# Performance work log

Hardware: AMD Instinct MI355X
Metric: run time of the kernel (lower is better)

Reference implementation:

```python
import jax, jax.numpy as jnp
import numpy as np
import math

B, T, C, H = 4, 1024, 1024, 16
D = C // H  # head dim = 64

def setup_inputs() -> dict:
    key = jax.random.key(0)
    ks = jax.random.split(key, 10)
    s = 1.0 / math.sqrt(C)
    x = jax.random.normal(ks[0], (B, T, C), dtype=jnp.float32)
    pad = (jax.random.uniform(ks[1], (B, T)) < 0.2).astype(jnp.float32)
    # ensure first token of every row is unpadded so softmax rows are well-posed
    pad = pad.at[:, 0].set(0.0)
    Wq = jax.random.normal(ks[2], (C, C), dtype=jnp.float32) * s
    bq = jnp.zeros((C,), dtype=jnp.float32)
    Wk = jax.random.normal(ks[3], (C, C), dtype=jnp.float32) * s
    bk = jnp.zeros((C,), dtype=jnp.float32)
    Wv = jax.random.normal(ks[4], (C, C), dtype=jnp.float32) * s
    bv = jnp.zeros((C,), dtype=jnp.float32)
    Wp = jax.random.normal(ks[5], (C, C), dtype=jnp.float32) * s
    bp = jnp.zeros((C,), dtype=jnp.float32)
    return {"x": x, "x_padding_judge": pad, "Wq": Wq, "bq": bq,
            "Wk": Wk, "bk": bk, "Wv": Wv, "bv": bv, "Wp": Wp, "bp": bp}

def reference(x, x_padding_judge, Wq, bq, Wk, bk, Wv, bv, Wp, bp):
    # keep flag: 1.0 where token is real, 0.0 where padded
    keep = 1.0 - x_padding_judge                      # [B, T]
    mask = keep[:, :, None] * keep[:, None, :]        # [B, T, T] outer product
    # projections, split heads: [B, H, T, D]
    def heads(w, b):
        return (x @ w + b).reshape(B, T, H, D).transpose(0, 2, 1, 3)
    q, k, v = heads(Wq, bq), heads(Wk, bk), heads(Wv, bv)
    att = jnp.einsum('bhqd,bhkd->bhqk', q, k) * (1.0 / math.sqrt(D))
    # attn_pdrop=0 => att_full is all ones; masked_fill where mask == 0
    att = jnp.where(mask[:, None, :, :] == 0, -1e9, att)
    att = jax.nn.softmax(att, axis=-1)
    y = jnp.einsum('bhqk,bhkd->bhqd', att, v)         # [B, H, T, D]
    y = y.transpose(0, 2, 1, 3).reshape(B, T, C)
    return y @ Wp + bp
```

## Files before the change

kernel.cpp:

```cpp
#include <hip/hip_runtime.h>
#include <hip/hip_bf16.h>
#include <math.h>

#define Bb 4
#define Tt 1024
#define Cc 1024
#define Hh 16
#define Dd 64

typedef __attribute__((ext_vector_type(8))) _Float16 half8;
typedef __attribute__((ext_vector_type(4))) _Float16 half4;
typedef __attribute__((ext_vector_type(4))) float floatx4;


__device__ __forceinline__ void gload_lds16(const _Float16* g, const _Float16* l)
{
    __builtin_amdgcn_global_load_lds(
        (const __attribute__((address_space(1))) void*)g,
        (__attribute__((address_space(3))) void*)l, 16, 0, 0);
}

struct PrepP { const float* x; _Float16* xh; const float* W[4]; _Float16* out[4]; };

__global__ __launch_bounds__(256) void prep_all(PrepP p)
{
    if (blockIdx.x < 256) {
        const int m16 = blockIdx.x;
        const int r   = threadIdx.x & 15;
        const int kc0 = threadIdx.x >> 4;
        const float* src = p.x + (size_t)(m16 * 16 + r) * 1024;
        _Float16*   dst = p.xh + (size_t)m16 * 16384 + r * 8;
#pragma unroll
        for (int c8 = 0; c8 < 8; ++c8) {
            const int kc = kc0 + c8 * 16;
            float4 a = *(const float4*)(src + kc * 8);
            float4 b = *(const float4*)(src + kc * 8 + 4);
            half8 h;
            h[0] = (_Float16)a.x; h[1] = (_Float16)a.y; h[2] = (_Float16)a.z; h[3] = (_Float16)a.w;
            h[4] = (_Float16)b.x; h[5] = (_Float16)b.y; h[6] = (_Float16)b.z; h[7] = (_Float16)b.w;
            *(half8*)(dst + kc * 128) = h;
        }
        return;
    }
    const int bid2 = blockIdx.x - 256;
    const int z    = bid2 >> 8;
    const int rem  = bid2 & 255;
    const int n0   = (rem & 15) * 64;
    const int k0   = (rem >> 4) * 64;
    const float* __restrict__ W = p.W[z];
    _Float16* __restrict__ outp = p.out[z];
    __shared__ float tile[64][65];
    const int tr  = threadIdx.x >> 4;
    const int tc4 = (threadIdx.x & 15) * 4;

#pragma unroll
    for (int i = 0; i < 4; ++i) {
        const int kk = tr + i * 16;
        float4 v = *(const float4*)(W + (size_t)(k0 + kk) * 1024 + n0 + tc4);
        tile[kk][tc4 + 0] = v.x;
        tile[kk][tc4 + 1] = v.y;
        tile[kk][tc4 + 2] = v.z;
        tile[kk][tc4 + 3] = v.w;
    }
    __syncthreads();
#pragma unroll
    for (int i = 0; i < 4; ++i) {
        half4 h;
#pragma unroll
        for (int c = 0; c < 4; ++c) h[c] = (_Float16)tile[tc4 + c][tr + i * 16];
        _Float16* dst = outp + (size_t)((n0 >> 4) + i) * 16384
                        + ((k0 + tc4) >> 3) * 128 + tr * 8 + (tc4 & 7);
        *(half4*)dst = h;
    }
}

struct QkvP { const _Float16* Wt[3]; const float* bias[3];
              _Float16* qb; _Float16* kb; _Float16* vt; };

#define QKV_STEP(CUR, SBUF, TS, DOSTAGE, TAILWAIT)                          \
    {                                                                       \
        half8 af[2], bf[4];                                                 \
        _Pragma("unroll")                                                   \
        for (int i = 0; i < 2; ++i)                                         \
            af[i] = *(const half8*)&As[CUR][wr * 2 + i][lane * 8];          \
        _Pragma("unroll")                                                   \
        for (int j = 0; j < 4; ++j)                                         \
            bf[j] = *(const half8*)&Bs[CUR][wc * 4 + j][lane * 8];          \
        if (DOSTAGE) {                                                      \
            const size_t ko = (size_t)(TS) * 512;                           \
            gload_lds16(ga + ko, &As[SBUF][w][0]);                          \
            gload_lds16(gb + ko, &Bs[SBUF][w][0]);                          \
        }                                                                   \
        _Pragma("unroll")                                                   \
        for (int i = 0; i < 2; ++i)                                         \
            _Pragma("unroll")                                               \
            for (int j = 0; j < 4; ++j)                                     \
                acc[i][j] = __builtin_amdgcn_mfma_f32_16x16x32_f16(         \
                    af[i], bf[j], acc[i][j], 0, 0, 0);                      \
        if ((TAILWAIT) == 2)                                                \
            asm volatile("s_waitcnt vmcnt(2)" ::: "memory");                \
        else if ((TAILWAIT) == 0)                                           \
            asm volatile("s_waitcnt vmcnt(0)" ::: "memory");                \
        if ((TAILWAIT) >= 0) __builtin_amdgcn_s_barrier();                  \
    }

__global__ __launch_bounds__(512) void gemm_qkv(const _Float16* __restrict__ xh, QkvP p)
{
    const int z = blockIdx.z;
    const _Float16* __restrict__ Wt   = p.Wt[z];
    const float* __restrict__    bias = p.bias[z];

    const int tid  = threadIdx.x;
    const int lane = tid & 63;
    const int w    = tid >> 6;
    const int wr   = w >> 1, wc = w & 1;
    const int quad = lane >> 4;
    const int l15  = lane & 15;
    const int bm   = blockIdx.x * 128;
    const int bn   = blockIdx.y * 128;

    __shared__ __align__(16) _Float16 As[3][8][512];
    __shared__ __align__(16) _Float16 Bs[3][8][512];

    const _Float16* ga = xh + (size_t)((bm >> 4) + w) * 16384 + lane * 8;
    const _Float16* gb = Wt + (size_t)((bn >> 4) + w) * 16384 + lane * 8;

    floatx4 acc[2][4];
#pragma unroll
    for (int i = 0; i < 2; ++i)
#pragma unroll
        for (int j = 0; j < 4; ++j)
            acc[i][j] = (floatx4){0.f, 0.f, 0.f, 0.f};

    gload_lds16(ga, &As[0][w][0]);
    gload_lds16(gb, &Bs[0][w][0]);
    gload_lds16(ga + 512, &As[1][w][0]);
    gload_lds16(gb + 512, &Bs[1][w][0]);
    asm volatile("s_waitcnt vmcnt(2)" ::: "memory");
    __builtin_amdgcn_s_barrier();

    for (int tt = 0; tt < 30; tt += 3) {
        QKV_STEP(0, 2, tt + 2, true, 2);
        QKV_STEP(1, 0, tt + 3, true, 2);
        QKV_STEP(2, 1, tt + 4, true, 2);
    }
    QKV_STEP(0, 0, 0, false, 0);
    QKV_STEP(1, 0, 0, false, -1);

    if (z == 2) {
#pragma unroll
        for (int j = 0; j < 4; ++j) {
            const int col = bn + wc * 64 + j * 16 + l15;
            const int h  = col >> 6;
            const float bj = bias[col];
#pragma unroll
            for (int i = 0; i < 2; ++i) {
                const int t0 = bm + wr * 32 + i * 16 + quad * 4;
                const int bh = (t0 >> 10) * 16 + h;
                const int tm = t0 & 1023;
                half4 pk;
#pragma unroll
                for (int r = 0; r < 4; ++r) pk[r] = (_Float16)(acc[i][j][r] + bj);
                *(half4*)(p.vt + (size_t)bh * 65536 + (size_t)j * 16384
                          + (tm >> 3) * 128 + l15 * 8 + (tm & 7)) = pk;
            }
        }
    } else {
        _Float16* outp = (z == 0) ? p.qb : p.kb;
#pragma unroll
        for (int j = 0; j < 4; ++j) {
            const int col = bn + wc * 64 + j * 16 + l15;
            const int h  = col >> 6;
            const int dd = col & 63;
            const float bj = bias[col];
            const int doff = (dd >> 3) * 128 + (dd & 7);
#pragma unroll
            for (int i = 0; i < 2; ++i) {
#pragma unroll
                for (int r = 0; r < 4; ++r) {
                    const int tg = bm + wr * 32 + i * 16 + quad * 4 + r;
                    const int bh = (tg >> 10) * 16 + h;
                    const int tm = tg & 1023;
                    outp[(size_t)bh * 65536 + (tm >> 4) * 1024 + doff + (tm & 15) * 8] =
                        (_Float16)(acc[i][j][r] + bj);
                }
            }
        }
    }
}

#define ATTN_TILE(AKC, BVC, AKN, BVN, KTC, KTN, DOLOAD)                     \
    {                                                                       \
        if (DOLOAD) {                                                       \
            _Pragma("unroll")                                               \
            for (int ks = 0; ks < 2; ++ks) {                                \
                _Pragma("unroll")                                           \
                for (int mk = 0; mk < 4; ++mk)                              \
                    AKN[ks][mk] = *(const half8*)(kf                        \
                        + (size_t)(((KTN) >> 4) + mk) * 1024                \
                        + ks * 512 + lane * 8);                             \
                _Pragma("unroll")                                           \
                for (int dj = 0; dj < 4; ++dj)                              \
                    BVN[ks][dj] = *(const half8*)(vf + (size_t)dj * 16384   \
                        + ((KTN) >> 3) * 128 + ks * 512 + lane * 8);        \
            }                                                               \
        }                                                                   \
        float4 kk4[4];                                                      \
        _Pragma("unroll")                                                   \
        for (int mk = 0; mk < 4; ++mk)                                      \
            kk4[mk] = *(const float4*)&Pad[(KTC) + mk * 16 + quad * 4];     \
        floatx4 ST[4][2];                                                   \
        _Pragma("unroll")                                                   \
        for (int mk = 0; mk < 4; ++mk)                                      \
            _Pragma("unroll")                                               \
            for (int nq = 0; nq < 2; ++nq)                                  \
                ST[mk][nq] = (floatx4){0.f, 0.f, 0.f, 0.f};                 \
        _Pragma("unroll")                                                   \
        for (int ks = 0; ks < 2; ++ks)                                      \
            _Pragma("unroll")                                               \
            for (int mk = 0; mk < 4; ++mk)                                  \
                _Pragma("unroll")                                           \
                for (int nq = 0; nq < 2; ++nq)                              \
                    ST[mk][nq] = __builtin_amdgcn_mfma_f32_16x16x32_f16(    \
                        AKC[ks][mk], bq[ks][nq], ST[mk][nq], 0, 0, 0);      \
        _Pragma("unroll")                                                   \
        for (int mk = 0; mk < 4; ++mk) {                                    \
            const float kkr[4] = {1.0f - kk4[mk].x, 1.0f - kk4[mk].y,       \
                                  1.0f - kk4[mk].z, 1.0f - kk4[mk].w};      \
            _Pragma("unroll")                                               \
            for (int nq = 0; nq < 2; ++nq) {                                \
                half4 pk;                                                   \
                _Pragma("unroll")                                           \
                for (int r = 0; r < 4; ++r) {                               \
                    const float e = __builtin_amdgcn_exp2f(ST[mk][nq][r] * SC); \
                    const float pv = (kq[nq] == 0.0f) ? 1.0f : kkr[r] * e;  \
                    pk[r] = (_Float16)pv;                                   \
                }                                                           \
                *(half4*)&Ps[w][((mk * 2 + (quad >> 1)) * 32 + nq * 16 + l15) * 8 \
                               + (quad & 1) * 4] = pk;                      \
            }                                                               \
        }                                                                   \
        _Pragma("unroll")                                                   \
        for (int ks = 0; ks < 2; ++ks) {                                    \
            half8 ap[2];                                                    \
            _Pragma("unroll")                                               \
            for (int mi = 0; mi < 2; ++mi)                                  \
                ap[mi] = *(const half8*)&Ps[w][((ks * 4 + quad) * 32 + mi * 16 + l15) * 8]; \
            _Pragma("unroll")                                               \
            for (int mi = 0; mi < 2; ++mi) {                                \
                _Pragma("unroll")                                           \
                for (int dj = 0; dj < 4; ++dj)                              \
                    O[mi][dj] = __builtin_amdgcn_mfma_f32_16x16x32_f16(     \
                        ap[mi], BVC[ks][dj], O[mi][dj], 0, 0, 0);           \
                l_acc[mi] = __builtin_amdgcn_mfma_f32_16x16x32_f16(         \
                    ap[mi], ones, l_acc[mi], 0, 0, 0);                      \
            }                                                               \
        }                                                                   \
    }

__global__ __launch_bounds__(256) void attn_mfma(
    const _Float16* __restrict__ qb, const _Float16* __restrict__ kb,
    const _Float16* __restrict__ vt, const float* __restrict__ padj,
    _Float16* __restrict__ yh)
{
    __shared__ __align__(16) _Float16 Ps[4][2048];
    __shared__ __align__(16) float    Pad[1024];

    const int tid  = threadIdx.x;
    const int lane = tid & 63;
    const int w    = tid >> 6;
    const int quad = lane >> 4;
    const int l15  = lane & 15;
    const int bh   = blockIdx.x;
    const int q0   = blockIdx.y * 128;
    const int b    = bh >> 4;
    const int h    = bh & 15;

    const _Float16* qf = qb + (size_t)bh * 65536;
    const _Float16* kf = kb + (size_t)bh * 65536;
    const _Float16* vf = vt + (size_t)bh * 65536;
    const float*    pk_row = padj + b * Tt;

    *(float4*)&Pad[tid * 4] = *(const float4*)(pk_row + tid * 4);

    half8 bq[2][2];
#pragma unroll
    for (int ks = 0; ks < 2; ++ks)
#pragma unroll
        for (int nq = 0; nq < 2; ++nq)
            bq[ks][nq] = *(const half8*)(qf + (size_t)((q0 >> 4) + w * 2 + nq) * 1024
                                         + ks * 512 + lane * 8);
    float kq[2];
#pragma unroll
    for (int nq = 0; nq < 2; ++nq)
        kq[nq] = 1.0f - pk_row[q0 + w * 32 + nq * 16 + l15];

    floatx4 O[2][4];
    floatx4 l_acc[2];
#pragma unroll
    for (int mi = 0; mi < 2; ++mi) {
#pragma unroll
        for (int dj = 0; dj < 4; ++dj) O[mi][dj] = (floatx4){0.f, 0.f, 0.f, 0.f};
        l_acc[mi] = (floatx4){0.f, 0.f, 0.f, 0.f};
    }
    half8 ones;
#pragma unroll
    for (int j = 0; j < 8; ++j) ones[j] = (_Float16)1.0f;

    constexpr float SC = 0.18033688011112042f;

    __syncthreads();

    half8 ak0[2][4], bv0[2][4], ak1[2][4], bv1[2][4];
#pragma unroll
    for (int ks = 0; ks < 2; ++ks) {
#pragma unroll
        for (int mk = 0; mk < 4; ++mk)
            ak0[ks][mk] = *(const half8*)(kf + (size_t)mk * 1024 + ks * 512 + lane * 8);
#pragma unroll
        for (int dj = 0; dj < 4; ++dj)
            bv0[ks][dj] = *(const half8*)(vf + (size_t)dj * 16384 + ks * 512 + lane * 8);
    }

    for (int tt = 0; tt < 896; tt += 128) {
        ATTN_TILE(ak0, bv0, ak1, bv1, tt, tt + 64, true);
        ATTN_TILE(ak1, bv1, ak0, bv0, tt + 64, tt + 128, true);
    }
    ATTN_TILE(ak0, bv0, ak1, bv1, 896, 960, true);
    ATTN_TILE(ak1, bv1, ak0, bv0, 960, 0, false);

#pragma unroll
    for (int mi = 0; mi < 2; ++mi) {
#pragma unroll
        for (int r = 0; r < 4; ++r) {
            const int rowl  = w * 32 + mi * 16 + quad * 4 + r;
            const int token = b * Tt + q0 + rowl;
            const float inv = 1.0f / l_acc[mi][r];
            const size_t tb = (size_t)(token >> 4) * 16384 + (token & 15) * 8;
#pragma unroll
            for (int dj = 0; dj < 4; ++dj) {
                const int col = h * 64 + dj * 16 + l15;
                yh[tb + (col >> 3) * 128 + (col & 7)] = (_Float16)(O[mi][dj][r] * inv);
            }
        }
    }
}

#define PROJ_STEP(CUR, SBUF, TS, DOSTAGE, TAILWAIT)                         \
    {                                                                       \
        half8 af[2], bf[4];                                                 \
        _Pragma("unroll")                                                   \
        for (int i = 0; i < 2; ++i)                                         \
            af[i] = *(const half8*)&As[CUR][wr * 2 + i][lane * 8];          \
        _Pragma("unroll")                                                   \
        for (int j = 0; j < 4; ++j)                                         \
            bf[j] = *(const half8*)&Bs[CUR][wc * 4 + j][lane * 8];          \
        if (DOSTAGE) {                                                      \
            const size_t ko = (size_t)(TS) * 512;                           \
            gload_lds16(ga + ko, &As[SBUF][w][0]);                          \
            gload_lds16(gb + ko, &Bs[SBUF][w][0]);                          \
        }                                                                   \
        _Pragma("unroll")                                                   \
        for (int i = 0; i < 2; ++i)                                         \
            _Pragma("unroll")                                               \
            for (int j = 0; j < 4; ++j)                                     \
                acc[i][j] = __builtin_amdgcn_mfma_f32_16x16x32_f16(         \
                    af[i], bf[j], acc[i][j], 0, 0, 0);                      \
        if ((TAILWAIT) == 6)                                                \
            asm volatile("s_waitcnt vmcnt(6)" ::: "memory");                \
        else if ((TAILWAIT) == 4)                                           \
            asm volatile("s_waitcnt vmcnt(4)" ::: "memory");                \
        else if ((TAILWAIT) == 2)                                           \
            asm volatile("s_waitcnt vmcnt(2)" ::: "memory");                \
        else if ((TAILWAIT) == 0)                                           \
            asm volatile("s_waitcnt vmcnt(0)" ::: "memory");                \
        if ((TAILWAIT) >= 0) __builtin_amdgcn_s_barrier();                  \
    }

__global__ __launch_bounds__(512) void gemm_proj(const _Float16* __restrict__ Ay,
                                                 const _Float16* __restrict__ Bt,
                                                 const float* __restrict__ bias,
                                                 float* __restrict__ out)
{
    const int tid  = threadIdx.x;
    const int lane = tid & 63;
    const int w    = tid >> 6;
    const int wr   = w >> 1, wc = w & 1;
    const int quad = lane >> 4;
    const int l15  = lane & 15;
    const int bm   = blockIdx.x * 128;
    const int bn   = blockIdx.y * 128;

    __shared__ __align__(16) _Float16 As[5][8][512];
    __shared__ __align__(16) _Float16 Bs[5][8][512];

    const _Float16* ga = Ay + (size_t)((bm >> 4) + w) * 16384 + lane * 8;
    const _Float16* gb = Bt + (size_t)((bn >> 4) + w) * 16384 + lane * 8;

    floatx4 acc[2][4];
#pragma unroll
    for (int i = 0; i < 2; ++i)
#pragma unroll
        for (int j = 0; j < 4; ++j)
            acc[i][j] = (floatx4){0.f, 0.f, 0.f, 0.f};

#pragma unroll
    for (int tb = 0; tb < 4; ++tb) {
        gload_lds16(ga + (size_t)tb * 512, &As[tb][w][0]);
        gload_lds16(gb + (size_t)tb * 512, &Bs[tb][w][0]);
    }
    asm volatile("s_waitcnt vmcnt(6)" ::: "memory");
    __builtin_amdgcn_s_barrier();

    for (int tt = 0; tt < 25; tt += 5) {
        PROJ_STEP(0, 4, tt + 4, true, 6);
        PROJ_STEP(1, 0, tt + 5, true, 6);
        PROJ_STEP(2, 1, tt + 6, true, 6);
        PROJ_STEP(3, 2, tt + 7, true, 6);
        PROJ_STEP(4, 3, tt + 8, true, 6);
    }
    PROJ_STEP(0, 4, 29, true, 6);
    PROJ_STEP(1, 0, 30, true, 6);
    PROJ_STEP(2, 1, 31, true, 6);
    PROJ_STEP(3, 0, 0, false, 4);
    PROJ_STEP(4, 0, 0, false, 2);
    PROJ_STEP(0, 0, 0, false, 0);
    PROJ_STEP(1, 0, 0, false, -1);

#pragma unroll
    for (int j = 0; j < 4; ++j) {
        const int col = bn + wc * 64 + j * 16 + l15;
        const float bj = bias[col];
#pragma unroll
        for (int i = 0; i < 2; ++i) {
            const int row = bm + wr * 32 + i * 16 + quad * 4;
            float* o = out + (size_t)row * 1024 + col;
#pragma unroll
            for (int r = 0; r < 4; ++r)
                o[(size_t)r * 1024] = acc[i][j][r] + bj;
        }
    }
}

extern "C" void kernel_launch(void* const* d_in, const int* in_sizes, int n_in,
                              void* d_out, int out_size, void* d_ws, size_t ws_size,
                              hipStream_t stream)
{
    const float* x    = (const float*)d_in[0];
    const float* padj = (const float*)d_in[1];
    const float* Wq   = (const float*)d_in[2];
    const float* bq   = (const float*)d_in[3];
    const float* Wk   = (const float*)d_in[4];
    const float* bk   = (const float*)d_in[5];
    const float* Wv   = (const float*)d_in[6];
    const float* bv   = (const float*)d_in[7];
    const float* Wp   = (const float*)d_in[8];
    const float* bp   = (const float*)d_in[9];
    float* out = (float*)d_out;

    const size_t MB = 1024 * 1024;
    char* ws = (char*)d_ws;
    _Float16* xh  = (_Float16*)(ws);
    _Float16* Wt0 = (_Float16*)(ws +  8 * MB);
    _Float16* Wt1 = (_Float16*)(ws + 10 * MB);
    _Float16* Wt2 = (_Float16*)(ws + 12 * MB);
    _Float16* Wtp = (_Float16*)(ws + 14 * MB);
    _Float16* qb  = (_Float16*)(ws + 16 * MB);
    _Float16* kb  = (_Float16*)(ws + 24 * MB);
    _Float16* vtb = (_Float16*)(ws + 32 * MB);
    _Float16* yh  = (_Float16*)(ws + 40 * MB);

    PrepP pp;
    pp.x = x; pp.xh = xh;
    pp.W[0] = Wq; pp.W[1] = Wk; pp.W[2] = Wv; pp.W[3] = Wp;
    pp.out[0] = Wt0; pp.out[1] = Wt1; pp.out[2] = Wt2; pp.out[3] = Wtp;
    prep_all<<<1280, 256, 0, stream>>>(pp);

    QkvP qp;
    qp.Wt[0] = Wt0; qp.Wt[1] = Wt1; qp.Wt[2] = Wt2;
    qp.bias[0] = bq; qp.bias[1] = bk; qp.bias[2] = bv;
    qp.qb = qb; qp.kb = kb; qp.vt = vtb;
    gemm_qkv<<<dim3(32, 8, 3), 512, 0, stream>>>(xh, qp);

    attn_mfma<<<dim3(64, 8), 256, 0, stream>>>(qb, kb, vtb, padj, yh);

    gemm_proj<<<dim3(32, 8), 512, 0, stream>>>(yh, Wtp, bp, out);
}
```

Baseline: 176.2 us.

## Halve attention query tile per wave to 16 rows and double the grid

Each wave in the attention kernel now handles 16 query rows instead of 32, so the block covers 64 queries and the grid doubles to 1024 blocks. Accumulator registers and LDS for P are halved, and launch bounds request 3 blocks per SM to raise occupancy and spread work across CUs. The cost is that every K/V fragment loaded from global memory is reused across half as many queries, doubling K/V traffic and per-tile overhead such as the exp/mask work per MFMA.

```diff
diff --git a/kernel.cpp b/kernel.cpp
--- a/kernel.cpp
+++ b/kernel.cpp
@@ -209,61 +209,48 @@
         _Pragma("unroll")                                                   \
         for (int mk = 0; mk < 4; ++mk)                                      \
             kk4[mk] = *(const float4*)&Pad[(KTC) + mk * 16 + quad * 4];     \
-        floatx4 ST[4][2];                                                   \
+        floatx4 ST[4];                                                      \
         _Pragma("unroll")                                                   \
         for (int mk = 0; mk < 4; ++mk)                                      \
-            _Pragma("unroll")                                               \
-            for (int nq = 0; nq < 2; ++nq)                                  \
-                ST[mk][nq] = (floatx4){0.f, 0.f, 0.f, 0.f};                 \
+            ST[mk] = (floatx4){0.f, 0.f, 0.f, 0.f};                         \
         _Pragma("unroll")                                                   \
         for (int ks = 0; ks < 2; ++ks)                                      \
             _Pragma("unroll")                                               \
             for (int mk = 0; mk < 4; ++mk)                                  \
-                _Pragma("unroll")                                           \
-                for (int nq = 0; nq < 2; ++nq)                              \
-                    ST[mk][nq] = __builtin_amdgcn_mfma_f32_16x16x32_f16(    \
-                        AKC[ks][mk], bq[ks][nq], ST[mk][nq], 0, 0, 0);      \
+                ST[mk] = __builtin_amdgcn_mfma_f32_16x16x32_f16(            \
+                    AKC[ks][mk], bq[ks], ST[mk], 0, 0, 0);                  \
         _Pragma("unroll")                                                   \
         for (int mk = 0; mk < 4; ++mk) {                                    \
             const float kkr[4] = {1.0f - kk4[mk].x, 1.0f - kk4[mk].y,       \
                                   1.0f - kk4[mk].z, 1.0f - kk4[mk].w};      \
-            _Pragma("unroll")                                               \
-            for (int nq = 0; nq < 2; ++nq) {                                \
-                half4 pk;                                                   \
-                _Pragma("unroll")                                           \
-                for (int r = 0; r < 4; ++r) {                               \
-                    const float e = __builtin_amdgcn_exp2f(ST[mk][nq][r] * SC); \
-                    const float pv = (kq[nq] == 0.0f) ? 1.0f : kkr[r] * e;  \
-                    pk[r] = (_Float16)pv;                                   \
-                }                                                           \
-                *(half4*)&Ps[w][((mk * 2 + (quad >> 1)) * 32 + nq * 16 + l15) * 8 \
-                               + (quad & 1) * 4] = pk;                      \
+            half4 pk;                                                       \
+            _Pragma("unroll")                                               \
+            for (int r = 0; r < 4; ++r) {                                   \
+                const float e = __builtin_amdgcn_exp2f(ST[mk][r] * SC);     \
+                const float pv = (kq == 0.0f) ? 1.0f : kkr[r] * e;          \
+                pk[r] = (_Float16)pv;                                       \
             }                                                               \
+            *(half4*)&Ps[w][((mk * 2 + (quad >> 1)) * 16 + l15) * 8         \
+                           + (quad & 1) * 4] = pk;                          \
         }                                                                   \
         _Pragma("unroll")                                                   \
         for (int ks = 0; ks < 2; ++ks) {                                    \
-            half8 ap[2];                                                    \
-            _Pragma("unroll")                                               \
-            for (int mi = 0; mi < 2; ++mi)                                  \
-                ap[mi] = *(const half8*)&Ps[w][((ks * 4 + quad) * 32 + mi * 16 + l15) * 8]; \
-            _Pragma("unroll")                                               \
-            for (int mi = 0; mi < 2; ++mi) {                                \
-                _Pragma("unroll")                                           \
-                for (int dj = 0; dj < 4; ++dj)                              \
-                    O[mi][dj] = __builtin_amdgcn_mfma_f32_16x16x32_f16(     \
-                        ap[mi], BVC[ks][dj], O[mi][dj], 0, 0, 0);           \
-                l_acc[mi] = __builtin_amdgcn_mfma_f32_16x16x32_f16(         \
-                    ap[mi], ones, l_acc[mi], 0, 0, 0);                      \
-            }                                                               \
+            half8 ap = *(const half8*)&Ps[w][((ks * 4 + quad) * 16 + l15) * 8]; \
+            _Pragma("unroll")                                               \
+            for (int dj = 0; dj < 4; ++dj)                                  \
+                O[dj] = __builtin_amdgcn_mfma_f32_16x16x32_f16(             \
+                    ap, BVC[ks][dj], O[dj], 0, 0, 0);                       \
+            l_acc = __builtin_amdgcn_mfma_f32_16x16x32_f16(                 \
+                ap, ones, l_acc, 0, 0, 0);                                  \
         }                                                                   \
     }
 
-__global__ __launch_bounds__(256) void attn_mfma(
+__global__ __launch_bounds__(256, 3) void attn_mfma(
     const _Float16* __restrict__ qb, const _Float16* __restrict__ kb,
     const _Float16* __restrict__ vt, const float* __restrict__ padj,
     _Float16* __restrict__ yh)
 {
-    __shared__ __align__(16) _Float16 Ps[4][2048];
+    __shared__ __align__(16) _Float16 Ps[4][1024];
     __shared__ __align__(16) float    Pad[1024];
 
     const int tid  = threadIdx.x;
@@ -272,7 +259,7 @@
     const int quad = lane >> 4;
     const int l15  = lane & 15;
     const int bh   = blockIdx.x;
-    const int q0   = blockIdx.y * 128;
+    const int q0   = blockIdx.y * 64;
     const int b    = bh >> 4;
     const int h    = bh & 15;
 
@@ -283,26 +270,18 @@
 
     *(float4*)&Pad[tid * 4] = *(const float4*)(pk_row + tid * 4);
 
-    half8 bq[2][2];
+    half8 bq[2];
 #pragma unroll
     for (int ks = 0; ks < 2; ++ks)
-#pragma unroll
-        for (int nq = 0; nq < 2; ++nq)
-            bq[ks][nq] = *(const half8*)(qf + (size_t)((q0 >> 4) + w * 2 + nq) * 1024
-                                         + ks * 512 + lane * 8);
-    float kq[2];
-#pragma unroll
-    for (int nq = 0; nq < 2; ++nq)
-        kq[nq] = 1.0f - pk_row[q0 + w * 32 + nq * 16 + l15];
-
-    floatx4 O[2][4];
-    floatx4 l_acc[2];
-#pragma unroll
-    for (int mi = 0; mi < 2; ++mi) {
-#pragma unroll
-        for (int dj = 0; dj < 4; ++dj) O[mi][dj] = (floatx4){0.f, 0.f, 0.f, 0.f};
-        l_acc[mi] = (floatx4){0.f, 0.f, 0.f, 0.f};
-    }
+        bq[ks] = *(const half8*)(qf + (size_t)((q0 >> 4) + w) * 1024
+                                 + ks * 512 + lane * 8);
+    const float kq = 1.0f - pk_row[q0 + w * 16 + l15];
+
+    floatx4 O[4];
+    floatx4 l_acc;
+#pragma unroll
+    for (int dj = 0; dj < 4; ++dj) O[dj] = (floatx4){0.f, 0.f, 0.f, 0.f};
+    l_acc = (floatx4){0.f, 0.f, 0.f, 0.f};
     half8 ones;
 #pragma unroll
     for (int j = 0; j < 8; ++j) ones[j] = (_Float16)1.0f;
@@ -330,18 +309,15 @@
     ATTN_TILE(ak1, bv1, ak0, bv0, 960, 0, false);
 
 #pragma unroll
-    for (int mi = 0; mi < 2; ++mi) {
-#pragma unroll
-        for (int r = 0; r < 4; ++r) {
-            const int rowl  = w * 32 + mi * 16 + quad * 4 + r;
-            const int token = b * Tt + q0 + rowl;
-            const float inv = 1.0f / l_acc[mi][r];
-            const size_t tb = (size_t)(token >> 4) * 16384 + (token & 15) * 8;
-#pragma unroll
-            for (int dj = 0; dj < 4; ++dj) {
-                const int col = h * 64 + dj * 16 + l15;
-                yh[tb + (col >> 3) * 128 + (col & 7)] = (_Float16)(O[mi][dj][r] * inv);
-            }
+    for (int r = 0; r < 4; ++r) {
+        const int rowl  = w * 16 + quad * 4 + r;
+        const int token = b * Tt + q0 + rowl;
+        const float inv = 1.0f / l_acc[r];
+        const size_t tb = (size_t)(token >> 4) * 16384 + (token & 15) * 8;
+#pragma unroll
+        for (int dj = 0; dj < 4; ++dj) {
+            const int col = h * 64 + dj * 16 + l15;
+            yh[tb + (col >> 3) * 128 + (col & 7)] = (_Float16)(O[dj][r] * inv);
         }
     }
 }
@@ -482,7 +458,7 @@
     qp.qb = qb; qp.kb = kb; qp.vt = vtb;
     gemm_qkv<<<dim3(32, 8, 3), 512, 0, stream>>>(xh, qp);
 
-    attn_mfma<<<dim3(64, 8), 256, 0, stream>>>(qb, kb, vtb, padj, yh);
+    attn_mfma<<<dim3(64, 16), 256, 0, stream>>>(qb, kb, vtb, padj, yh);
 
     gemm_proj<<<dim3(32, 8), 512, 0, stream>>>(yh, Wtp, bp, out);
 }
```

After: 219.1 us. 1.24x slower.
